# Kernel optimization log

Measured on AMD Instinct MI355X. Metric: run time of the kernel, lower is better.

## Reference

```python
import jax, jax.numpy as jnp
import numpy as np

B, M, N, C, H = 2, 2048, 2048, 1024, 16
HD = C // H  # head dim = 64


def setup_inputs() -> dict:
    key = jax.random.key(0)
    ks = jax.random.split(key, 8)
    std = 0.25
    return {
        "x": jax.random.normal(ks[0], (B, M, C), dtype=jnp.float32),
        "data": jax.random.normal(ks[1], (B, N, C), dtype=jnp.float32),
        # weights stored [in, out] (transpose of torch Linear weight)
        "W_attn": jax.random.normal(ks[2], (C, 3 * C), dtype=jnp.float32) * std,
        "b_attn": jnp.zeros((3 * C,), dtype=jnp.float32),
        "W_data": jax.random.normal(ks[3], (C, 2 * C), dtype=jnp.float32) * std,
        "b_data": jnp.zeros((2 * C,), dtype=jnp.float32),
        "W_proj": jax.random.normal(ks[4], (C, C), dtype=jnp.float32) * std,
        "b_proj": jnp.zeros((C,), dtype=jnp.float32),
    }


def reference(x, data, W_attn, b_attn, W_data, b_data, W_proj, b_proj):
    # QKV from queries x: [B, M, 3, C] -> q, k, v each [B, M, C]
    qkv = (x @ W_attn + b_attn).reshape(B, M, 3, C)
    q, k, v = qkv[:, :, 0], qkv[:, :, 1], qkv[:, :, 2]
    # KV from data: [B, N, 2, C]
    kv = (data @ W_data + b_data).reshape(B, N, 2, C)
    k_data, v_data = kv[:, :, 0], kv[:, :, 1]
    # concat self KV with data KV along sequence -> length T = M + N
    k = jnp.concatenate([k, k_data], axis=1)
    v = jnp.concatenate([v, v_data], axis=1)
    T = M + N
    # split heads
    qh = q.reshape(B, M, H, HD).transpose(0, 2, 1, 3)  # [B,H,M,HD]
    kh = k.reshape(B, T, H, HD).transpose(0, 2, 1, 3)  # [B,H,T,HD]
    vh = v.reshape(B, T, H, HD).transpose(0, 2, 1, 3)  # [B,H,T,HD]
    scale = 1.0 / np.sqrt(HD).astype(np.float32)
    attn = jax.nn.softmax(jnp.einsum("bhmd,bhtd->bhmt", qh, kh) * scale, axis=-1)
    out = jnp.einsum("bhmt,bhtd->bhmd", attn, vh)  # [B,H,M,HD]
    out = out.transpose(0, 2, 1, 3).reshape(B, M, C)
    return out @ W_proj + b_proj
```

## Files before the change

### kernel.cpp

```cpp
#include <hip/hip_runtime.h>

typedef __bf16 bf16x8 __attribute__((ext_vector_type(8)));
typedef __bf16 bf16x4 __attribute__((ext_vector_type(4)));
typedef _Float16 f16x8 __attribute__((ext_vector_type(8)));
typedef float f32x4 __attribute__((ext_vector_type(4)));
typedef float f32x16 __attribute__((ext_vector_type(16)));
typedef unsigned short u16x8 __attribute__((ext_vector_type(8)));
typedef unsigned short u16x4 __attribute__((ext_vector_type(4)));
typedef unsigned int u32x4 __attribute__((ext_vector_type(4)));
typedef unsigned short us;

#define MM 2048
#define TT 4096

__device__ __forceinline__ us f2bf(float f){
  unsigned int u = __builtin_bit_cast(unsigned int, f);
  u = (u + 0x7fffu + ((u >> 16) & 1u)) >> 16;
  return (us)u;
}
__device__ __forceinline__ float bf2f(us u){
  unsigned int x = ((unsigned int)u) << 16;
  return __builtin_bit_cast(float, x);
}
__device__ __forceinline__ us f2h(float f){
  _Float16 h = (_Float16)f;
  return __builtin_bit_cast(us, h);
}
__device__ __forceinline__ unsigned int cvt_pk_bf16(float lo, float hi){
  unsigned int r;
  asm("v_cvt_pk_bf16_f32 %0, %1, %2" : "=v"(r) : "v"(lo), "v"(hi));
  return r;
}
__device__ __forceinline__ void plane_swap(unsigned int &x, unsigned int &y){
  asm("v_permlane32_swap_b32 %0, %1" : "+v"(x), "+v"(y));
}
__device__ __forceinline__ float fast_exp2(float s, float A23, float B23){
  float t = __builtin_fmaf(s, A23, B23);
  unsigned int u;
  asm("v_cvt_u32_f32 %0, %1" : "=v"(u) : "v"(t));
  return __builtin_bit_cast(float, u);
}

#define GLDS(gp, lp) __builtin_amdgcn_global_load_lds( \
    (const __attribute__((address_space(1))) unsigned int*)(gp), \
    (__attribute__((address_space(3))) unsigned int*)(lp), 16, 0, 0)

__global__ __launch_bounds__(256) void prep_all(const float* __restrict__ x,
                                                const float* __restrict__ data,
                                                const float* __restrict__ W_attn,
                                                const float* __restrict__ W_data,
                                                const float* __restrict__ W_proj,
                                                us* __restrict__ xf, us* __restrict__ df,
                                                us* __restrict__ Af, us* __restrict__ Df,
                                                us* __restrict__ Pb){
  __shared__ float tile[32][33];
  int bid = blockIdx.x;
  if (bid < 4096){
    const float* in; us* o;
    if (bid < 2048){ in = x; o = xf; }
    else           { in = data; o = df; bid -= 2048; }
    size_t i = ((size_t)bid * 256 + threadIdx.x) * 8;
    float4 a = *(const float4*)(in + i);
    float4 b = *(const float4*)(in + i + 4);
    float v[8] = {a.x,a.y,a.z,a.w,b.x,b.y,b.z,b.w};
    u16x8 r;
    for (int j = 0; j < 8; j++) r[j] = f2h(v[j]);
    *(u16x8*)(o + i) = r;
    return;
  }
  int blk = bid - 4096;
  int bx = blk % 192;
  int k0 = (blk / 192) * 32;
  const float* W; us* o; int N; bool tobf;
  if (bx < 96){ W = W_attn; o = Af; N = 3072; tobf = false; }
  else if (bx < 160){ W = W_data; o = Df; N = 2048; bx -= 96; tobf = false; }
  else { W = W_proj; o = Pb; N = 1024; bx -= 160; tobf = true; }
  int tx = threadIdx.x & 31, ty = threadIdx.x >> 5;
  int n0 = bx * 32;
  for (int r = 0; r < 32; r += 8)
    tile[ty + r][tx] = W[(size_t)(k0 + ty + r) * N + n0 + tx];
  __syncthreads();
  for (int r = 0; r < 32; r += 8){
    float v = tile[tx][ty + r];
    size_t idx = (size_t)(n0 + ty + r) * 1024 + k0 + tx;
    o[idx] = tobf ? f2bf(v) : f2h(v);
  }
}

__global__ __launch_bounds__(256) void gemm_all(const us* __restrict__ xf, const us* __restrict__ df,
                                                const us* __restrict__ Watf, const us* __restrict__ Wdtf,
                                                const float* __restrict__ b_attn, const float* __restrict__ b_data,
                                                us* __restrict__ Qf, us* __restrict__ Kf,
                                                us* __restrict__ VT){
  __shared__ us shm[16640];
  us* sm = shm;
  const int bx = blockIdx.x;
  const us *Ah, *Bth; const float* bias; int region, kroff, col0;
  if (bx < 24){
    Ah = xf; Bth = Watf; bias = b_attn;
    region = bx >> 3; kroff = 0; col0 = bx * 128;
  } else {
    int b2 = bx - 24;
    Ah = df; Bth = Wdtf; bias = b_data;
    region = 1 + (b2 >> 3); kroff = 2048; col0 = b2 * 128;
  }
  const int tid = threadIdx.x, wid = tid >> 6, lane = tid & 63;
  const int l15 = lane & 15, l16 = lane >> 4;
  const int row0 = blockIdx.y * 128;
  const int wr = (wid >> 1) * 64, wc = (wid & 1) * 64;
  f32x4 acc[4][4] = {};

  for (int k0 = 0; k0 < 1024; k0 += 32){
    for (int c = 0; c < 2; ++c){
      int i = c * 256 + tid;
      size_t aoff = (size_t)(row0 + (i >> 2)) * 1024 + k0 + (i & 3) * 8;
      size_t boff = (size_t)(col0 + (i >> 2)) * 1024 + k0 + (i & 3) * 8;
      GLDS(Ah + aoff, &sm[c * 2048 + wid * 512]);
      GLDS(Bth + boff, &sm[4096 + c * 2048 + wid * 512]);
    }
    __syncthreads();
    f16x8 af[4], bf[4];
    for (int m = 0; m < 4; m++) af[m] = *(const f16x8*)&sm[(wr + m * 16 + l15) * 32 + l16 * 8];
    for (int n = 0; n < 4; n++) bf[n] = *(const f16x8*)&sm[4096 + (wc + n * 16 + l15) * 32 + l16 * 8];
    for (int m = 0; m < 4; m++)
      for (int n = 0; n < 4; n++)
        acc[m][n] = __builtin_amdgcn_mfma_f32_16x16x32_f16(af[m], bf[n], acc[m][n], 0, 0, 0);
    __syncthreads();
  }

  if (region == 2){
    us* Tv = &shm[wid * 4160];
    for (int m = 0; m < 4; m++)
      for (int n = 0; n < 4; n++){
        float bv = bias[col0 + wc + n * 16 + l15];
        for (int j = 0; j < 4; j++)
          Tv[(m * 16 + l16 * 4 + j) * 65 + n * 16 + l15] = f2bf(acc[m][n][j] + bv);
      }
    __syncthreads();
    const int b2r = (row0 + wr) >> 11;
    const int t64 = kroff + ((row0 + wr) & 2047);
    const int d0  = (col0 + wc) & 1023;
    const int dl  = lane >> 2, tl = (lane & 3) * 16;
#pragma unroll
    for (int p = 0; p < 4; p++){
      int dloc = p * 16 + dl;
      u16x8 w0, w1;
#pragma unroll
      for (int i = 0; i < 8; i++){
        w0[i] = Tv[(tl + i) * 65 + dloc];
        w1[i] = Tv[(tl + 8 + i) * 65 + dloc];
      }
      us* dst = &VT[((size_t)(b2r * 1024 + d0 + dloc)) * 4096 + t64 + tl];
      *(u16x8*)dst = w0;
      *(u16x8*)(dst + 8) = w1;
    }
  } else {
    for (int m = 0; m < 4; m++)
      for (int n = 0; n < 4; n++){
        int gcol = col0 + wc + n * 16 + l15;
        int ocol = gcol & 1023;
        float bv = bias[gcol];
        us* P = (region == 0) ? Qf : Kf;
        for (int j = 0; j < 4; j++){
          int r = row0 + wr + m * 16 + l16 * 4 + j;
          size_t orow = (region == 0) ? (size_t)r
                                      : (size_t)((r >> 11) * 4096 + kroff + (r & 2047));
          P[orow * 1024 + ocol] = f2h(acc[m][n][j] + bv);
        }
      }
  }
}

__global__ __launch_bounds__(256) void gemm_proj(const us* __restrict__ Ah,
                                                 const us* __restrict__ Bth,
                                                 const float* __restrict__ bias,
                                                 float* __restrict__ Co){
  __shared__ us sm[12288];
  const int tid = threadIdx.x, wid = tid >> 6, lane = tid & 63;
  const int l15 = lane & 15, l16 = lane >> 4;
  const int row0 = blockIdx.y * 128, col0 = blockIdx.x * 64;
  const int wr = (wid >> 1) * 64, wc = (wid & 1) * 32;
  f32x4 acc[4][2] = {};

  for (int k0 = 0; k0 < 1024; k0 += 32){
    for (int c = 0; c < 2; ++c){
      int i = c * 256 + tid;
      size_t aoff = (size_t)(row0 + (i >> 2)) * 1024 + k0 + (i & 3) * 8;
      GLDS(Ah + aoff, &sm[c * 2048 + wid * 512]);
    }
    {
      size_t boff = (size_t)(col0 + (tid >> 2)) * 1024 + k0 + (tid & 3) * 8;
      GLDS(Bth + boff, &sm[8192 + wid * 512]);
    }
    __syncthreads();
    bf16x8 afh[4], bfh[2];
    for (int m = 0; m < 4; m++) afh[m] = *(const bf16x8*)&sm[(wr + m * 16 + l15) * 32 + l16 * 8];
    for (int n = 0; n < 2; n++) bfh[n] = *(const bf16x8*)&sm[8192 + (wc + n * 16 + l15) * 32 + l16 * 8];
    for (int m = 0; m < 4; m++)
      for (int n = 0; n < 2; n++)
        acc[m][n] = __builtin_amdgcn_mfma_f32_16x16x32_bf16(afh[m], bfh[n], acc[m][n], 0, 0, 0);
    __syncthreads();
  }

  for (int m = 0; m < 4; m++)
    for (int n = 0; n < 2; n++){
      int col = col0 + wc + n * 16 + l15;
      float bv = bias[col];
      for (int j = 0; j < 4; j++){
        int r = row0 + wr + m * 16 + l16 * 4 + j;
        Co[(size_t)r * 1024 + col] = acc[m][n][j] + bv;
      }
    }
}

__global__ __launch_bounds__(256, 4) void attn_kernel(const us* __restrict__ Qf,
                                                      const us* __restrict__ Kf,
                                                      const us* __restrict__ VT,
                                                      us* __restrict__ accP,
                                                      float* __restrict__ Mv, float* __restrict__ Lv){
  __shared__ us Kb[2][64 * 72];
  __shared__ us Vb[2][64 * 72];
  const int tid = threadIdx.x, wid = tid >> 6, lane = tid & 63;
  const int l31 = lane & 31, hb = lane >> 5, h8 = hb * 8;
  const int bid = blockIdx.x;
  const int swz = (bid & 7) * 128 + (bid >> 3);
  const int qt = swz & 15;
  const int bh = (swz >> 4) & 31;
  const int tch = swz >> 9;
  const int hd = (bh & 15) * 64, b = bh >> 4;
  const int qrow = qt * 128 + wid * 32 + l31;
  const int tbase = tch * 2048, tend = tbase + 2048;

  f16x8 qf[4];
  {
    const us* qp = Qf + (size_t)(b * MM + qrow) * 1024 + hd;
#pragma unroll
    for (int kk = 0; kk < 4; kk++)
      qf[kk] = *(const f16x8*)(qp + kk * 16 + h8);
  }

  u16x8 ones_u;
#pragma unroll
  for (int j = 0; j < 8; j++) ones_u[j] = 0x3F80;
  const bf16x8 ones8 = __builtin_bit_cast(bf16x8, ones_u);

  const int i0 = tid, i1 = 256 + tid;
  const int kt0 = i0 >> 3, kd0 = (i0 & 7) * 8;
  const int kt1 = i1 >> 3, kd1 = (i1 & 7) * 8;

#define GK(t0_, t_, d_) (((size_t)(b * TT + (t0_) + (t_))) * 1024 + hd + (d_))
#define GV(t0_, d_, t_) (((size_t)b * 1024 + hd + (d_)) * 4096 + (t0_) + (t_))

  uint4 rK0 = *(const uint4*)(Kf + GK(tbase, kt0, kd0));
  uint4 rK1 = *(const uint4*)(Kf + GK(tbase, kt1, kd1));
  uint4 rV0 = *(const uint4*)(VT + GV(tbase, kt0, kd0));
  uint4 rV1 = *(const uint4*)(VT + GV(tbase, kt1, kd1));
  *(uint4*)&Kb[0][kt0 * 72 + kd0] = rK0;
  *(uint4*)&Kb[0][kt1 * 72 + kd1] = rK1;
  *(uint4*)&Vb[0][kt0 * 72 + kd0] = rV0;
  *(uint4*)&Vb[0][kt1 * 72 + kd1] = rV1;
  __syncthreads();

  const us* pK0 = Kf + GK(tbase + 64, kt0, kd0);
  const us* pK1 = Kf + GK(tbase + 64, kt1, kd1);
  const us* pV0 = VT + GV(tbase + 64, kt0, kd0);
  const us* pV1 = VT + GV(tbase + 64, kt1, kd1);

  f32x16 acc0 = {}, acc1 = {}, accS = {};
  float mrow = -1e30f;
  const float cs  = 0.125f * 1.44269504088896f;
  const float A23 = cs * 8388608.0f;
  float B23 = 0.f;

  for (int t0 = tbase; t0 < tend; t0 += 64){
    const int cur = (t0 >> 6) & 1;
    const bool pre = (t0 + 64 < tend);
    if (pre){
      rK0 = *(const uint4*)pK0; pK0 += 64 * 1024;
      rK1 = *(const uint4*)pK1; pK1 += 64 * 1024;
      rV0 = *(const uint4*)pV0; pV0 += 64;
      rV1 = *(const uint4*)pV1; pV1 += 64;
    }

    const us* KbC = &Kb[cur][0];
    f32x16 sfr0 = {}, sfr1 = {};
    __builtin_amdgcn_s_setprio(1);
#pragma unroll
    for (int kk = 0; kk < 4; kk++){
      f16x8 a0 = *(const f16x8*)&KbC[l31 * 72 + kk * 16 + h8];
      f16x8 a1 = *(const f16x8*)&KbC[(32 + l31) * 72 + kk * 16 + h8];
      sfr0 = __builtin_amdgcn_mfma_f32_32x32x16_f16(a0, qf[kk], sfr0, 0, 0, 0);
      sfr1 = __builtin_amdgcn_mfma_f32_32x32x16_f16(a1, qf[kk], sfr1, 0, 0, 0);
    }
    __builtin_amdgcn_s_setprio(0);

    float va = -1e30f, vb2 = -1e30f;
#pragma unroll
    for (int r = 0; r < 16; r += 2){
      va  = fmaxf(fmaxf(sfr0[r],     sfr1[r]),     va);
      vb2 = fmaxf(fmaxf(sfr0[r + 1], sfr1[r + 1]), vb2);
    }
    float v = fmaxf(va, vb2);
    float vs = v * cs;
    vs = fmaxf(vs, __shfl_xor(vs, 32, 64));
    if (!__all(vs <= mrow + 8.f)){
      float mn = fmaxf(mrow, vs);
      float rs = __builtin_amdgcn_exp2f(mrow - mn);
      mrow = mn;
      B23 = __builtin_fmaf(mrow, -8388608.0f, 1065103216.0f);
#pragma unroll
      for (int r = 0; r < 16; r++){ acc0[r] *= rs; acc1[r] *= rs; accS[r] *= rs; }
    }
    unsigned int A0[4][2], A1[4][2];
#pragma unroll
    for (int g = 0; g < 4; g++){
      float e00 = fast_exp2(sfr0[4*g+0], A23, B23);
      float e01 = fast_exp2(sfr0[4*g+1], A23, B23);
      float e02 = fast_exp2(sfr0[4*g+2], A23, B23);
      float e03 = fast_exp2(sfr0[4*g+3], A23, B23);
      float e10 = fast_exp2(sfr1[4*g+0], A23, B23);
      float e11 = fast_exp2(sfr1[4*g+1], A23, B23);
      float e12 = fast_exp2(sfr1[4*g+2], A23, B23);
      float e13 = fast_exp2(sfr1[4*g+3], A23, B23);
      A0[g][0] = cvt_pk_bf16(e00, e01);
      A0[g][1] = cvt_pk_bf16(e02, e03);
      A1[g][0] = cvt_pk_bf16(e10, e11);
      A1[g][1] = cvt_pk_bf16(e12, e13);
    }

    bf16x8 pf[4];
#pragma unroll
    for (int kkl = 0; kkl < 2; kkl++){
      unsigned int x0 = A0[2*kkl][0], y0 = A0[2*kkl+1][0];
      unsigned int x1 = A0[2*kkl][1], y1 = A0[2*kkl+1][1];
      plane_swap(x0, y0);
      plane_swap(x1, y1);
      u32x4 w = {x0, x1, y0, y1};
      pf[kkl] = __builtin_bit_cast(bf16x8, w);
      unsigned int z0 = A1[2*kkl][0], t0w = A1[2*kkl+1][0];
      unsigned int z1 = A1[2*kkl][1], t1w = A1[2*kkl+1][1];
      plane_swap(z0, t0w);
      plane_swap(z1, t1w);
      u32x4 w2 = {z0, z1, t0w, t1w};
      pf[2 + kkl] = __builtin_bit_cast(bf16x8, w2);
    }

    const us* VbC = &Vb[cur][0];
    __builtin_amdgcn_s_setprio(1);
#pragma unroll
    for (int kk = 0; kk < 4; kk++){
      bf16x8 av0 = *(const bf16x8*)&VbC[l31 * 72 + kk * 16 + h8];
      bf16x8 av1 = *(const bf16x8*)&VbC[(32 + l31) * 72 + kk * 16 + h8];
      acc0 = __builtin_amdgcn_mfma_f32_32x32x16_bf16(av0, pf[kk], acc0, 0, 0, 0);
      acc1 = __builtin_amdgcn_mfma_f32_32x32x16_bf16(av1, pf[kk], acc1, 0, 0, 0);
      accS = __builtin_amdgcn_mfma_f32_32x32x16_bf16(ones8, pf[kk], accS, 0, 0, 0);
    }
    __builtin_amdgcn_s_setprio(0);

    if (pre){
      const int nxt = cur ^ 1;
      *(uint4*)&Kb[nxt][kt0 * 72 + kd0] = rK0;
      *(uint4*)&Kb[nxt][kt1 * 72 + kd1] = rK1;
      *(uint4*)&Vb[nxt][kt0 * 72 + kd0] = rV0;
      *(uint4*)&Vb[nxt][kt1 * 72 + kd1] = rV1;
    }
    __syncthreads();
  }
#undef GK
#undef GV

  us* ap = accP + (size_t)tch * 4194304 + (size_t)(b * MM + qrow) * 1024 + hd;
#pragma unroll
  for (int g = 0; g < 4; g++){
    bf16x4 w0, w1;
#pragma unroll
    for (int j = 0; j < 4; j++){
      w0[j] = (__bf16)acc0[4 * g + j];
      w1[j] = (__bf16)acc1[4 * g + j];
    }
    *(u16x4*)&ap[8 * g + 4 * hb]      = __builtin_bit_cast(u16x4, w0);
    *(u16x4*)&ap[32 + 8 * g + 4 * hb] = __builtin_bit_cast(u16x4, w1);
  }
  if (hb == 0){
    int idx = tch * 65536 + (b * MM + qrow) * 16 + (hd >> 6);
    Mv[idx] = mrow;
    Lv[idx] = accS[0];
  }
}

__global__ __launch_bounds__(256) void combine_kernel(const us* __restrict__ accP,
                                                      const float* __restrict__ Mv,
                                                      const float* __restrict__ Lv,
                                                      us* __restrict__ attno){
  size_t i = ((size_t)blockIdx.x * 256 + threadIdx.x) * 8;
  size_t qg = i >> 10;
  int h = (int)((i & 1023) >> 6);
  size_t mi = qg * 16 + h;
  float m1 = Mv[mi], m2 = Mv[65536 + mi];
  float l1 = Lv[mi], l2 = Lv[65536 + mi];
  float m = fmaxf(m1, m2);
  float w1 = __builtin_amdgcn_exp2f(m1 - m);
  float w2 = __builtin_amdgcn_exp2f(m2 - m);
  float inv = 1.f / (w1 * l1 + w2 * l2);
  float s1 = w1 * inv, s2 = w2 * inv;
  u16x8 a1 = *(const u16x8*)(accP + i);
  u16x8 a2 = *(const u16x8*)(accP + 4194304 + i);
  u16x8 o;
#pragma unroll
  for (int j = 0; j < 8; j++)
    o[j] = f2bf(s1 * bf2f(a1[j]) + s2 * bf2f(a2[j]));
  *(u16x8*)(attno + i) = o;
}

extern "C" void kernel_launch(void* const* d_in, const int* in_sizes, int n_in,
                              void* d_out, int out_size, void* d_ws, size_t ws_size,
                              hipStream_t stream){
  const float* x      = (const float*)d_in[0];
  const float* data   = (const float*)d_in[1];
  const float* W_attn = (const float*)d_in[2];
  const float* b_attn = (const float*)d_in[3];
  const float* W_data = (const float*)d_in[4];
  const float* b_data = (const float*)d_in[5];
  const float* W_proj = (const float*)d_in[6];
  const float* b_proj = (const float*)d_in[7];
  float* out = (float*)d_out;

  char* ws = (char*)d_ws;
  us* xf    = (us*)(ws + 0);
  us* df    = (us*)(ws + 8388608);
  us* Watf  = (us*)(ws + 16777216);
  us* Wdtf  = (us*)(ws + 23068672);
  us* Wptb  = (us*)(ws + 27262976);
  us* Qf    = (us*)(ws + 29360128);
  us* Kf    = (us*)(ws + 37748736);
  us* VT    = (us*)(ws + 54525952);
  us* accP  = (us*)(ws + 71303168);
  float* Mv = (float*)(ws + 88080384);
  float* Lv = (float*)(ws + 88604672);
  us* attno = (us*)(ws + 0);

  prep_all<<<10240, 256, 0, stream>>>(x, data, W_attn, W_data, W_proj,
                                      xf, df, Watf, Wdtf, Wptb);

  gemm_all<<<dim3(40, 32), 256, 0, stream>>>(xf, df, Watf, Wdtf,
                                             b_attn, b_data, Qf, Kf, VT);

  attn_kernel<<<1024, 256, 0, stream>>>(Qf, Kf, VT, accP, Mv, Lv);
  combine_kernel<<<2048, 256, 0, stream>>>(accP, Mv, Lv, attno);

  gemm_proj<<<dim3(16, 32), 256, 0, stream>>>(attno, Wptb, b_proj, out);
}
```

Measured before the change: 214.7 us.

## Fuse split-KV combine into attention kernel via in-block LDS exchange

Attention now runs 512-thread blocks in which two 256-thread subgroups each handle one half of the key sequence for the same query tile. They merge their partial outputs and softmax statistics through shared memory instead of writing bf16 partials to global memory and launching a separate combine kernel. This removes one kernel launch, the global round-trip of the partial accumulators, and the bf16 rounding of the partials. In exchange the grid is halved to 512 blocks, block-wide syncs now span 8 waves, and shared memory per block grows to 72 KB, which may limit occupancy.

```diff
diff --git a/kernel.cpp b/kernel.cpp
--- a/kernel.cpp
+++ b/kernel.cpp
@@ -213,23 +213,26 @@
     }
 }
 
-__global__ __launch_bounds__(256, 4) void attn_kernel(const us* __restrict__ Qf,
+__global__ __launch_bounds__(512, 4) void attn_kernel(const us* __restrict__ Qf,
                                                       const us* __restrict__ Kf,
                                                       const us* __restrict__ VT,
-                                                      us* __restrict__ accP,
-                                                      float* __restrict__ Mv, float* __restrict__ Lv){
-  __shared__ us Kb[2][64 * 72];
-  __shared__ us Vb[2][64 * 72];
-  const int tid = threadIdx.x, wid = tid >> 6, lane = tid & 63;
+                                                      us* __restrict__ attno){
+  __shared__ uint4 shq[4608];
+  us* const base = (us*)shq;
+  const int tid = threadIdx.x;
+  const int sg = tid >> 8;
+  const int stid = tid & 255;
+  const int wid = stid >> 6, lane = tid & 63;
   const int l31 = lane & 31, hb = lane >> 5, h8 = hb * 8;
   const int bid = blockIdx.x;
-  const int swz = (bid & 7) * 128 + (bid >> 3);
+  const int swz = (bid & 7) * 64 + (bid >> 3);
   const int qt = swz & 15;
-  const int bh = (swz >> 4) & 31;
-  const int tch = swz >> 9;
+  const int bh = swz >> 4;
   const int hd = (bh & 15) * 64, b = bh >> 4;
   const int qrow = qt * 128 + wid * 32 + l31;
-  const int tbase = tch * 2048, tend = tbase + 2048;
+  const int tbase = sg * 2048, tend = tbase + 2048;
+  us* const KbS = base + sg * 9216;
+  us* const VbS = base + 18432 + sg * 9216;
 
   f16x8 qf[4];
   {
@@ -244,7 +247,7 @@
   for (int j = 0; j < 8; j++) ones_u[j] = 0x3F80;
   const bf16x8 ones8 = __builtin_bit_cast(bf16x8, ones_u);
 
-  const int i0 = tid, i1 = 256 + tid;
+  const int i0 = stid, i1 = 256 + stid;
   const int kt0 = i0 >> 3, kd0 = (i0 & 7) * 8;
   const int kt1 = i1 >> 3, kd1 = (i1 & 7) * 8;
 
@@ -255,10 +258,10 @@
   uint4 rK1 = *(const uint4*)(Kf + GK(tbase, kt1, kd1));
   uint4 rV0 = *(const uint4*)(VT + GV(tbase, kt0, kd0));
   uint4 rV1 = *(const uint4*)(VT + GV(tbase, kt1, kd1));
-  *(uint4*)&Kb[0][kt0 * 72 + kd0] = rK0;
-  *(uint4*)&Kb[0][kt1 * 72 + kd1] = rK1;
-  *(uint4*)&Vb[0][kt0 * 72 + kd0] = rV0;
-  *(uint4*)&Vb[0][kt1 * 72 + kd1] = rV1;
+  *(uint4*)&KbS[kt0 * 72 + kd0] = rK0;
+  *(uint4*)&KbS[kt1 * 72 + kd1] = rK1;
+  *(uint4*)&VbS[kt0 * 72 + kd0] = rV0;
+  *(uint4*)&VbS[kt1 * 72 + kd1] = rV1;
   __syncthreads();
 
   const us* pK0 = Kf + GK(tbase + 64, kt0, kd0);
@@ -282,7 +285,7 @@
       rV1 = *(const uint4*)pV1; pV1 += 64;
     }
 
-    const us* KbC = &Kb[cur][0];
+    const us* KbC = KbS + cur * 4608;
     f32x16 sfr0 = {}, sfr1 = {};
     __builtin_amdgcn_s_setprio(1);
 #pragma unroll
@@ -345,7 +348,7 @@
       pf[2 + kkl] = __builtin_bit_cast(bf16x8, w2);
     }
 
-    const us* VbC = &Vb[cur][0];
+    const us* VbC = VbS + cur * 4608;
     __builtin_amdgcn_s_setprio(1);
 #pragma unroll
     for (int kk = 0; kk < 4; kk++){
@@ -359,57 +362,52 @@
 
     if (pre){
       const int nxt = cur ^ 1;
-      *(uint4*)&Kb[nxt][kt0 * 72 + kd0] = rK0;
-      *(uint4*)&Kb[nxt][kt1 * 72 + kd1] = rK1;
-      *(uint4*)&Vb[nxt][kt0 * 72 + kd0] = rV0;
-      *(uint4*)&Vb[nxt][kt1 * 72 + kd1] = rV1;
+      *(uint4*)&KbS[nxt * 4608 + kt0 * 72 + kd0] = rK0;
+      *(uint4*)&KbS[nxt * 4608 + kt1 * 72 + kd1] = rK1;
+      *(uint4*)&VbS[nxt * 4608 + kt0 * 72 + kd0] = rV0;
+      *(uint4*)&VbS[nxt * 4608 + kt1 * 72 + kd1] = rV1;
     }
     __syncthreads();
   }
 #undef GK
 #undef GV
 
-  us* ap = accP + (size_t)tch * 4194304 + (size_t)(b * MM + qrow) * 1024 + hd;
-#pragma unroll
-  for (int g = 0; g < 4; g++){
-    bf16x4 w0, w1;
-#pragma unroll
-    for (int j = 0; j < 4; j++){
-      w0[j] = (__bf16)acc0[4 * g + j];
-      w1[j] = (__bf16)acc1[4 * g + j];
-    }
-    *(u16x4*)&ap[8 * g + 4 * hb]      = __builtin_bit_cast(u16x4, w0);
-    *(u16x4*)&ap[32 + 8 * g + 4 * hb] = __builtin_bit_cast(u16x4, w1);
-  }
-  if (hb == 0){
-    int idx = tch * 65536 + (b * MM + qrow) * 16 + (hd >> 6);
-    Mv[idx] = mrow;
-    Lv[idx] = accS[0];
-  }
-}
-
-__global__ __launch_bounds__(256) void combine_kernel(const us* __restrict__ accP,
-                                                      const float* __restrict__ Mv,
-                                                      const float* __restrict__ Lv,
-                                                      us* __restrict__ attno){
-  size_t i = ((size_t)blockIdx.x * 256 + threadIdx.x) * 8;
-  size_t qg = i >> 10;
-  int h = (int)((i & 1023) >> 6);
-  size_t mi = qg * 16 + h;
-  float m1 = Mv[mi], m2 = Mv[65536 + mi];
-  float l1 = Lv[mi], l2 = Lv[65536 + mi];
-  float m = fmaxf(m1, m2);
-  float w1 = __builtin_amdgcn_exp2f(m1 - m);
-  float w2 = __builtin_amdgcn_exp2f(m2 - m);
-  float inv = 1.f / (w1 * l1 + w2 * l2);
-  float s1 = w1 * inv, s2 = w2 * inv;
-  u16x8 a1 = *(const u16x8*)(accP + i);
-  u16x8 a2 = *(const u16x8*)(accP + 4194304 + i);
-  u16x8 o;
-#pragma unroll
-  for (int j = 0; j < 8; j++)
-    o[j] = f2bf(s1 * bf2f(a1[j]) + s2 * bf2f(a2[j]));
-  *(u16x8*)(attno + i) = o;
+  float* const ex   = (float*)shq;
+  float* const exml = ((float*)shq) + 8192;
+  if (sg == 1){
+#pragma unroll
+    for (int r = 0; r < 16; r++){
+      ex[(wid * 64 + lane) * 32 + r]      = acc0[r];
+      ex[(wid * 64 + lane) * 32 + 16 + r] = acc1[r];
+    }
+    if (hb == 0){
+      exml[(wid * 32 + l31) * 2]     = mrow;
+      exml[(wid * 32 + l31) * 2 + 1] = accS[0];
+    }
+  }
+  __syncthreads();
+  if (sg == 0){
+    float m1  = exml[(wid * 32 + l31) * 2];
+    float l1v = exml[(wid * 32 + l31) * 2 + 1];
+    float m = fmaxf(mrow, m1);
+    float w0s = __builtin_amdgcn_exp2f(mrow - m);
+    float w1s = __builtin_amdgcn_exp2f(m1 - m);
+    float inv = 1.f / (w0s * accS[0] + w1s * l1v);
+    float c0 = w0s * inv, c1 = w1s * inv;
+    const float* exp_ = &ex[(wid * 64 + lane) * 32];
+    us* op = attno + (size_t)(b * MM + qrow) * 1024 + hd;
+#pragma unroll
+    for (int g = 0; g < 4; g++){
+      bf16x4 w0v, w1v;
+#pragma unroll
+      for (int j = 0; j < 4; j++){
+        w0v[j] = (__bf16)(c0 * acc0[4 * g + j] + c1 * exp_[4 * g + j]);
+        w1v[j] = (__bf16)(c0 * acc1[4 * g + j] + c1 * exp_[16 + 4 * g + j]);
+      }
+      *(u16x4*)&op[8 * g + 4 * hb]      = __builtin_bit_cast(u16x4, w0v);
+      *(u16x4*)&op[32 + 8 * g + 4 * hb] = __builtin_bit_cast(u16x4, w1v);
+    }
+  }
 }
 
 extern "C" void kernel_launch(void* const* d_in, const int* in_sizes, int n_in,
@@ -434,9 +432,6 @@
   us* Qf    = (us*)(ws + 29360128);
   us* Kf    = (us*)(ws + 37748736);
   us* VT    = (us*)(ws + 54525952);
-  us* accP  = (us*)(ws + 71303168);
-  float* Mv = (float*)(ws + 88080384);
-  float* Lv = (float*)(ws + 88604672);
   us* attno = (us*)(ws + 0);
 
   prep_all<<<10240, 256, 0, stream>>>(x, data, W_attn, W_data, W_proj,
@@ -445,8 +440,7 @@
   gemm_all<<<dim3(40, 32), 256, 0, stream>>>(xf, df, Watf, Wdtf,
                                              b_attn, b_data, Qf, Kf, VT);
 
-  attn_kernel<<<1024, 256, 0, stream>>>(Qf, Kf, VT, accP, Mv, Lv);
-  combine_kernel<<<2048, 256, 0, stream>>>(accP, Mv, Lv, attno);
+  attn_kernel<<<512, 512, 0, stream>>>(Qf, Kf, VT, attno);
 
   gemm_proj<<<dim3(16, 32), 256, 0, stream>>>(attno, Wptb, b_proj, out);
 }
```

Result: no change. 217.3 us (+1.2%).
